# Optimization experiments

Hardware: AMD Instinct MI355X
Metric: run time of the kernel (lower is better)

## Reference

```python
import jax, jax.numpy as jnp
import numpy as np

N_LAYERS = 6
N_HEADS = 16
HIDDEN = 1024
HEAD = HIDDEN // N_HEADS  # 64
FFWD = 4096
VOCAB = 32000
WIN = 512
EMBED = 128
BATCH = 4
NEG_INF = -1.0e9


def layer_norm(x, bias, scale, eps=1e-6):
    m = jnp.mean(x, axis=-1, keepdims=True)
    v = jnp.mean(jnp.square(x - m), axis=-1, keepdims=True)
    return (x - m) * jax.lax.rsqrt(v + eps) * scale + bias


def setup_inputs() -> dict:
    key = jax.random.key(0)
    ks = jax.random.split(key, 16)

    def rn(k, shape):
        return 0.1 * jax.random.normal(k, shape, jnp.float32)

    return {
        "x_input": jax.random.randint(ks[0], (BATCH, WIN), 0, VOCAB),
        "prev_inputs": jax.random.normal(ks[1], (N_LAYERS, BATCH, WIN, HIDDEN), jnp.float32),
        "W_emb_dec": rn(ks[2], (VOCAB, EMBED)),
        "W_dec_lin": rn(ks[3], (EMBED, HIDDEN)),
        "p_decoder": rn(ks[4], (HIDDEN, VOCAB)),
        "p_d_q": rn(ks[5], (N_LAYERS, HIDDEN, HIDDEN)),
        "p_d_k": rn(ks[6], (N_LAYERS, HIDDEN, HIDDEN)),
        "p_d_v": rn(ks[7], (N_LAYERS, HIDDEN, HIDDEN)),
        "p_d_c": rn(ks[8], (N_LAYERS, HIDDEN, HIDDEN)),
        "p_d_ff1": rn(ks[9], (N_LAYERS, HIDDEN, FFWD)),
        "p_d_ff2": rn(ks[10], (N_LAYERS, FFWD, HIDDEN)),
        "b_d_ff1": jnp.zeros((N_LAYERS, FFWD), jnp.float32),
        "b_d_ff2": jnp.zeros((N_LAYERS, HIDDEN), jnp.float32),
        "b_d_bias_1": jnp.zeros((N_LAYERS, HIDDEN), jnp.float32),
        "b_d_bias_2": jnp.zeros((N_LAYERS, HIDDEN), jnp.float32),
        "b_d_scale_1": jnp.ones((N_LAYERS, HIDDEN), jnp.float32),
        "b_d_scale_2": jnp.ones((N_LAYERS, HIDDEN), jnp.float32),
        "x_emb_pos_dec": rn(ks[11], (N_LAYERS, 2 * WIN, HIDDEN)),
    }


def reference(x_input, prev_inputs, W_emb_dec, W_dec_lin, p_decoder,
              p_d_q, p_d_k, p_d_v, p_d_c, p_d_ff1, p_d_ff2,
              b_d_ff1, b_d_ff2, b_d_bias_1, b_d_bias_2,
              b_d_scale_1, b_d_scale_2, x_emb_pos_dec):
    L = x_input.shape[1]
    # token embedding (scaled by 1/sqrt(hidden)) then linear to hidden
    tok = W_emb_dec[x_input] * (HIDDEN ** -0.5)        # [B, L, E]
    h0 = jnp.einsum('ble,eh->blh', tok, W_dec_lin)     # [B, L, H]

    mask_len = L + WIN
    mask = NEG_INF * (1.0 - jnp.tril(jnp.ones((mask_len, mask_len), jnp.float32)))

    def split_heads(x):
        b, t, _ = x.shape
        return x.reshape(b, t, N_HEADS, HEAD).transpose(0, 2, 1, 3)  # [B, nH, T, d]

    def layer_fn(layer_input, p):
        Wq, Wk, Wv, Wc, Wf1, Wf2, bf1, bf2, b1, s1, b2, s2, pos, prev = p
        # concat cached window with current input, add positional embedding
        x = pos[None] + jnp.concatenate([prev, layer_input], axis=1)  # [B, 2W, H]
        q = split_heads(x @ Wq) * (HEAD ** -0.5)
        k = split_heads(x @ Wk)
        v = split_heads(x @ Wv)
        scores = jnp.einsum('bhqd,bhkd->bhqk', q, k) + mask
        alphas = jax.nn.softmax(scores, axis=-1)
        o = jnp.einsum('bhqk,bhkd->bhqd', alphas, v)
        o = o.transpose(0, 2, 1, 3).reshape(x.shape)  # combine heads
        attn = o @ Wc
        # var_type == 'norm_add': residual + LN(sublayer)
        x_self = x + layer_norm(attn, b1, s1)
        ff = jnp.maximum(x_self @ Wf1 + bf1, 0.0) @ Wf2 + bf2
        y = x_self + layer_norm(ff, b2, s2)
        new = y[:, WIN:, :]  # drop the cached-window positions
        return new, new

    params = (p_d_q, p_d_k, p_d_v, p_d_c, p_d_ff1, p_d_ff2,
              b_d_ff1, b_d_ff2, b_d_bias_1, b_d_scale_1,
              b_d_bias_2, b_d_scale_2, x_emb_pos_dec, prev_inputs)
    _, dec_outputs = jax.lax.scan(layer_fn, h0, params)  # [n_layers, B, L, H]
    dec_logits = jnp.einsum('blh,hv->blv', dec_outputs[-1], p_decoder)
    return (dec_logits, dec_outputs)
```

## Files before the change

kernel.cpp:

```cpp
#include <hip/hip_runtime.h>
#include <hip/hip_bf16.h>

#define NL   6
#define NH   16
#define HID  1024
#define HD   64
#define FFW  4096
#define VOC  32000
#define WINN 512
#define EMB  128
#define NB   4
#define TT   1024

typedef __attribute__((ext_vector_type(8))) _Float16 f16x8;
typedef __attribute__((ext_vector_type(8))) short    b16x8;
typedef __attribute__((ext_vector_type(4))) float    f32x4;

__device__ __forceinline__ ushort f2b(float f) {
    __hip_bfloat16 h = __float2bfloat16(f);
    return *reinterpret_cast<ushort*>(&h);
}
__device__ __forceinline__ void split16(float f, ushort& hb, ushort& lb) {
    _Float16 h = (_Float16)f;
    _Float16 l = (_Float16)((f - (float)h) * 2048.0f);
    hb = __builtin_bit_cast(ushort, h);
    lb = __builtin_bit_cast(ushort, l);
}
__device__ __forceinline__ void gload16(const void* g, void* l) {
    __builtin_amdgcn_global_load_lds(
        (const __attribute__((address_space(1))) unsigned int*)g,
        (__attribute__((address_space(3))) unsigned int*)l, 16, 0, 0);
}

__global__ __launch_bounds__(256) void embed_kernel(
    const int* __restrict__ xin, const float* __restrict__ Wemb,
    const float* __restrict__ Wlin, float* __restrict__ h0)
{
    int row = blockIdx.x;
    int tok = xin[row];
    __shared__ float tk[EMB];
    if (threadIdx.x < EMB) tk[threadIdx.x] = Wemb[tok * EMB + threadIdx.x] * 0.03125f;
    __syncthreads();
    for (int j = 0; j < 4; ++j) {
        int c = threadIdx.x + 256 * j;
        float acc = 0.f;
        for (int e = 0; e < EMB; ++e) acc += tk[e] * Wlin[e * HID + c];
        h0[(long)row * HID + c] = acc;
    }
}

__global__ __launch_bounds__(256) void build_x_kernel(
    const float* __restrict__ pos, const float* __restrict__ prev,
    const float* __restrict__ cur, float* __restrict__ x,
    ushort* __restrict__ xh, ushort* __restrict__ xl)
{
    int i4 = blockIdx.x * blockDim.x + threadIdx.x;
    if (i4 >= NB * TT * HID / 4) return;
    int h4 = i4 % (HID / 4);
    int bt = i4 / (HID / 4);
    int t = bt % TT, b = bt / TT;
    float4 p = ((const float4*)pos)[t * (HID / 4) + h4];
    float4 s;
    if (t < WINN) s = ((const float4*)prev)[(long)(b * WINN + t) * (HID / 4) + h4];
    else          s = ((const float4*)cur)[(long)(b * WINN + (t - WINN)) * (HID / 4) + h4];
    float4 r; r.x = p.x + s.x; r.y = p.y + s.y; r.z = p.z + s.z; r.w = p.w + s.w;
    ((float4*)x)[i4] = r;
    ushort4 uh, ul;
    split16(r.x, uh.x, ul.x); split16(r.y, uh.y, ul.y);
    split16(r.z, uh.z, ul.z); split16(r.w, uh.w, ul.w);
    ((ushort4*)xh)[i4] = uh;
    ((ushort4*)xl)[i4] = ul;
}

__global__ __launch_bounds__(256) void wsplit_kernel(
    const float* __restrict__ W, ushort* __restrict__ Wth, ushort* __restrict__ Wtl,
    int K, int N)
{
    __shared__ float ts[32][33];
    int n0 = blockIdx.x * 32, k0 = blockIdx.y * 32;
    int tr = threadIdx.x >> 5, tc = threadIdx.x & 31;
#pragma unroll
    for (int j = 0; j < 4; ++j)
        ts[tr + j * 8][tc] = W[(long)(k0 + tr + j * 8) * N + n0 + tc];
    __syncthreads();
#pragma unroll
    for (int j = 0; j < 4; ++j) {
        int n = tr + j * 8;
        ushort hb, lb;
        split16(ts[tc][n], hb, lb);
        long idx = (long)(n0 + n) * K + k0 + tc;
        Wth[idx] = hb;
        Wtl[idx] = lb;
    }
}

__global__ __launch_bounds__(256) void wsplit4_kernel(
    const float* __restrict__ pq, const float* __restrict__ pk,
    const float* __restrict__ pv, const float* __restrict__ pc,
    ushort* __restrict__ wq_h, ushort* __restrict__ wq_l,
    ushort* __restrict__ wkv_h, ushort* __restrict__ wkv_l,
    ushort* __restrict__ wc_h, ushort* __restrict__ wc_l)
{
    const float* src; ushort* dh; ushort* dl;
    switch (blockIdx.z) {
        case 0:  src = pq; dh = wq_h;            dl = wq_l;            break;
        case 1:  src = pk; dh = wkv_h;           dl = wkv_l;           break;
        case 2:  src = pv; dh = wkv_h + 1048576; dl = wkv_l + 1048576; break;
        default: src = pc; dh = wc_h;            dl = wc_l;            break;
    }
    __shared__ float ts[32][33];
    int n0 = blockIdx.x * 32, k0 = blockIdx.y * 32;
    int tr = threadIdx.x >> 5, tc = threadIdx.x & 31;
#pragma unroll
    for (int j = 0; j < 4; ++j)
        ts[tr + j * 8][tc] = src[(long)(k0 + tr + j * 8) * HID + n0 + tc];
    __syncthreads();
#pragma unroll
    for (int j = 0; j < 4; ++j) {
        int n = tr + j * 8;
        ushort hb, lb;
        split16(ts[tc][n], hb, lb);
        long idx = (long)(n0 + n) * HID + k0 + tc;
        dh[idx] = hb;
        dl[idx] = lb;
    }
}

__global__ __launch_bounds__(256) void vtrans_kernel(
    const ushort* __restrict__ vh, const ushort* __restrict__ vl,
    ushort* __restrict__ vth, ushort* __restrict__ vtl, int src_stride)
{
    __shared__ ushort th[32][33], tl[32][33];
    int n0 = blockIdx.x * 32, r0 = blockIdx.y * 32;
    int tr = threadIdx.x >> 5, tc = threadIdx.x & 31;
#pragma unroll
    for (int j = 0; j < 4; ++j) {
        long g = (long)(r0 + tr + j * 8) * src_stride + n0 + tc;
        th[tr + j * 8][tc] = vh[g];
        tl[tr + j * 8][tc] = vl[g];
    }
    __syncthreads();
#pragma unroll
    for (int j = 0; j < 4; ++j) {
        long g = (long)(n0 + tr + j * 8) * (NB * TT) + r0 + tc;
        vth[g] = th[tc][tr + j * 8];
        vtl[g] = tl[tc][tr + j * 8];
    }
}

__global__ __launch_bounds__(512) void hgemm8(
    const ushort* __restrict__ Ah, const ushort* __restrict__ Al,
    const ushort* __restrict__ Bh, const ushort* __restrict__ Bl,
    ushort* __restrict__ Chh, ushort* __restrict__ Cll,
    float* __restrict__ Cf0, float* __restrict__ Cf1,
    float* __restrict__ Cf2, float* __restrict__ Cf3,
    int M, int N, int K_stride, int Ksub,
    float scale, const float* __restrict__ bias, int relu, int amap)
{
    __shared__ __align__(16) ushort Ash[128 * 32];
    __shared__ __align__(16) ushort Asl[128 * 32];
    __shared__ __align__(16) ushort Bsh[128 * 32];
    __shared__ __align__(16) ushort Bsl[128 * 32];
    const int tid  = threadIdx.x;
    const int rb   = blockIdx.y * 128;
    const int cb   = blockIdx.x * 128;
    const int z    = blockIdx.z;
    const int k_off = z * Ksub;
    const int wave = tid >> 6, lane = tid & 63;
    const int wr   = (wave >> 2) * 64;
    const int wc   = (wave & 3) * 32;
    const int lr   = lane & 15;
    const int kh   = lane >> 4;

    const int lrow = lane >> 2;
    const int lkc  = (lane & 3) * 8;
    int gra = rb + wave * 16 + lrow;
    long marow = amap ? (long)((gra >> 9) * 1024 + 512 + (gra & 511)) : (long)gra;
    const ushort* gA_h = Ah + marow * K_stride + k_off + lkc;
    const ushort* gA_l = Al + marow * K_stride + k_off + lkc;
    const ushort* gB_h = Bh + (long)(cb + wave * 16 + lrow) * K_stride + k_off + lkc;
    const ushort* gB_l = Bl + (long)(cb + wave * 16 + lrow) * K_stride + k_off + lkc;
    ushort* lA_h = Ash + wave * 512;
    ushort* lA_l = Asl + wave * 512;
    ushort* lB_h = Bsh + wave * 512;
    ushort* lB_l = Bsl + wave * 512;

    int aoff[4], boff[2];
#pragma unroll
    for (int m = 0; m < 4; ++m) aoff[m] = (wr + m * 16 + lr) * 32 + kh * 8;
#pragma unroll
    for (int n = 0; n < 2; ++n) boff[n] = (wc + n * 16 + lr) * 32 + kh * 8;

    f32x4 accH[4][2], accL[4][2];
#pragma unroll
    for (int m = 0; m < 4; ++m)
#pragma unroll
        for (int n = 0; n < 2; ++n) {
            accH[m][n] = (f32x4){0.f, 0.f, 0.f, 0.f};
            accL[m][n] = (f32x4){0.f, 0.f, 0.f, 0.f};
        }

    for (int k0 = 0; k0 < Ksub; k0 += 32) {
        __syncthreads();
        gload16(gA_h + k0, lA_h);
        gload16(gA_l + k0, lA_l);
        gload16(gB_h + k0, lB_h);
        gload16(gB_l + k0, lB_l);
        __syncthreads();
        f16x8 afh[4], afl[4], bfh[2], bfl[2];
#pragma unroll
        for (int m = 0; m < 4; ++m) {
            afh[m] = *(const f16x8*)(Ash + aoff[m]);
            afl[m] = *(const f16x8*)(Asl + aoff[m]);
        }
#pragma unroll
        for (int n = 0; n < 2; ++n) {
            bfh[n] = *(const f16x8*)(Bsh + boff[n]);
            bfl[n] = *(const f16x8*)(Bsl + boff[n]);
        }
#pragma unroll
        for (int m = 0; m < 4; ++m)
#pragma unroll
            for (int n = 0; n < 2; ++n) {
                accH[m][n] = __builtin_amdgcn_mfma_f32_16x16x32_f16(afh[m], bfh[n], accH[m][n], 0, 0, 0);
                accL[m][n] = __builtin_amdgcn_mfma_f32_16x16x32_f16(afh[m], bfl[n], accL[m][n], 0, 0, 0);
                accL[m][n] = __builtin_amdgcn_mfma_f32_16x16x32_f16(afl[m], bfh[n], accL[m][n], 0, 0, 0);
            }
    }

    if (Cf0) {
        float* __restrict__ Cf = (z == 0) ? Cf0 : (z == 1) ? Cf1 : (z == 2) ? Cf2 : Cf3;
        const float* bias_eff = (z == 0) ? bias : nullptr;
#pragma unroll
        for (int m = 0; m < 4; ++m) {
            int row0 = rb + wr + m * 16 + kh * 4;
#pragma unroll
            for (int n = 0; n < 2; ++n) {
                int col = cb + wc + n * 16 + lr;
                float bv = bias_eff ? bias_eff[col] : 0.f;
#pragma unroll
                for (int r = 0; r < 4; ++r) {
                    float v = (accH[m][n][r] + accL[m][n][r] * (1.f / 2048.f)) * scale + bv;
                    if (relu) v = fmaxf(v, 0.f);
                    Cf[(long)(row0 + r) * N + col] = v;
                }
            }
        }
    } else {
#pragma unroll
        for (int m = 0; m < 4; ++m) {
            int row0 = rb + wr + m * 16 + kh * 4;
#pragma unroll
            for (int n = 0; n < 2; ++n) {
                int col = cb + wc + n * 16 + lr;
                float bv = bias ? bias[col] : 0.f;
#pragma unroll
                for (int r = 0; r < 4; ++r) {
                    float v = (accH[m][n][r] + accL[m][n][r] * (1.f / 2048.f)) * scale + bv;
                    if (relu) v = fmaxf(v, 0.f);
                    long idx = (long)(row0 + r) * N + col;
                    ushort hb, lb; split16(v, hb, lb);
                    Chh[idx] = hb; Cll[idx] = lb;
                }
            }
        }
    }
}

__global__ __launch_bounds__(256) void fattn_mfma(
    const float* __restrict__ qa, const float* __restrict__ qb,
    const float* __restrict__ qc, const float* __restrict__ qd,
    const ushort* __restrict__ kbh, const ushort* __restrict__ kbl, int kstr,
    const ushort* __restrict__ vth, const ushort* __restrict__ vtl,
    ushort* __restrict__ oh, ushort* __restrict__ ol)
{
    __shared__ __align__(16) ushort ksh[64 * 72];
    __shared__ __align__(16) ushort ksl[64 * 72];
    __shared__ __align__(16) ushort vsh[64 * 72];
    __shared__ __align__(16) ushort vsl[64 * 72];
    const int qt = blockIdx.x, h = blockIdx.y, b = blockIdx.z;
    const int tid = threadIdx.x;
    const int wave = tid >> 6, lane = tid & 63;
    const int lr = lane & 15, kg4 = lane >> 4;
    const int qbase = b * WINN + qt * 64;

    f16x8 qfh[2], qfl[2];
#pragma unroll
    for (int c = 0; c < 2; ++c) {
        long ga = (long)(qbase + wave * 16 + lr) * HID + h * HD + c * 32 + kg4 * 8;
        float4 a0 = *(const float4*)(qa + ga);
        float4 a1 = *(const float4*)(qa + ga + 4);
        float4 b0 = *(const float4*)(qb + ga);
        float4 b1 = *(const float4*)(qb + ga + 4);
        float4 c0 = *(const float4*)(qc + ga);
        float4 c1 = *(const float4*)(qc + ga + 4);
        float4 d0 = *(const float4*)(qd + ga);
        float4 d1 = *(const float4*)(qd + ga + 4);
        float qv[8] = {a0.x + b0.x + c0.x + d0.x, a0.y + b0.y + c0.y + d0.y,
                       a0.z + b0.z + c0.z + d0.z, a0.w + b0.w + c0.w + d0.w,
                       a1.x + b1.x + c1.x + d1.x, a1.y + b1.y + c1.y + d1.y,
                       a1.z + b1.z + c1.z + d1.z, a1.w + b1.w + c1.w + d1.w};
        ushort uh[8], ul[8];
#pragma unroll
        for (int j = 0; j < 8; ++j) split16(qv[j], uh[j], ul[j]);
        qfh[c] = *(const f16x8*)uh;
        qfl[c] = *(const f16x8*)ul;
    }

    f32x4 accOH[4], accOL[4];
#pragma unroll
    for (int d = 0; d < 4; ++d) {
        accOH[d] = (f32x4){0.f, 0.f, 0.f, 0.f};
        accOL[d] = (f32x4){0.f, 0.f, 0.f, 0.f};
    }
    float mrow[4], lrow[4];
#pragma unroll
    for (int r = 0; r < 4; ++r) { mrow[r] = -3.0e38f; lrow[r] = 0.f; }

    const int sr = tid >> 2;
    const int sd = (tid & 3) * 16;

    uint4 rk0, rk1, rk2, rk3, rv0, rv1, rv2, rv3;
    {
        long gk = (long)(b * TT + sr) * kstr + h * HD + sd;
        rk0 = *(const uint4*)(kbh + gk); rk1 = *(const uint4*)(kbh + gk + 8);
        rk2 = *(const uint4*)(kbl + gk); rk3 = *(const uint4*)(kbl + gk + 8);
        long gv = (long)(h * HD + sr) * (NB * TT) + b * TT + sd;
        rv0 = *(const uint4*)(vth + gv); rv1 = *(const uint4*)(vth + gv + 8);
        rv2 = *(const uint4*)(vtl + gv); rv3 = *(const uint4*)(vtl + gv + 8);
    }

    const int ktmax = 9 + qt;
    for (int kt = 0; kt < ktmax; ++kt) {
        __syncthreads();
        *(uint4*)(ksh + sr * 72 + sd) = rk0;
        *(uint4*)(ksh + sr * 72 + sd + 8) = rk1;
        *(uint4*)(ksl + sr * 72 + sd) = rk2;
        *(uint4*)(ksl + sr * 72 + sd + 8) = rk3;
        *(uint4*)(vsh + sr * 72 + sd) = rv0;
        *(uint4*)(vsh + sr * 72 + sd + 8) = rv1;
        *(uint4*)(vsl + sr * 72 + sd) = rv2;
        *(uint4*)(vsl + sr * 72 + sd + 8) = rv3;
        __syncthreads();

        f32x4 sH[4], sL[4];
#pragma unroll
        for (int n = 0; n < 4; ++n) {
            sH[n] = (f32x4){0.f, 0.f, 0.f, 0.f};
            sL[n] = (f32x4){0.f, 0.f, 0.f, 0.f};
        }
#pragma unroll
        for (int c = 0; c < 2; ++c) {
#pragma unroll
            for (int n = 0; n < 4; ++n) {
                int ad = (n * 16 + lr) * 72 + c * 32 + kg4 * 8;
                f16x8 bh = *(const f16x8*)(ksh + ad);
                f16x8 bl = *(const f16x8*)(ksl + ad);
                sH[n] = __builtin_amdgcn_mfma_f32_16x16x32_f16(qfh[c], bh, sH[n], 0, 0, 0);
                sL[n] = __builtin_amdgcn_mfma_f32_16x16x32_f16(qfh[c], bl, sL[n], 0, 0, 0);
                sL[n] = __builtin_amdgcn_mfma_f32_16x16x32_f16(qfl[c], bh, sL[n], 0, 0, 0);
            }
        }

        if (kt + 1 < ktmax) {
            long gk = (long)(b * TT + (kt + 1) * 64 + sr) * kstr + h * HD + sd;
            rk0 = *(const uint4*)(kbh + gk); rk1 = *(const uint4*)(kbh + gk + 8);
            rk2 = *(const uint4*)(kbl + gk); rk3 = *(const uint4*)(kbl + gk + 8);
            long gv = (long)(h * HD + sr) * (NB * TT) + b * TT + (kt + 1) * 64 + sd;
            rv0 = *(const uint4*)(vth + gv); rv1 = *(const uint4*)(vth + gv + 8);
            rv2 = *(const uint4*)(vtl + gv); rv3 = *(const uint4*)(vtl + gv + 8);
        }

        float S[4][4];
#pragma unroll
        for (int n = 0; n < 4; ++n)
#pragma unroll
            for (int r = 0; r < 4; ++r)
                S[n][r] = sH[n][r] + sL[n][r] * (1.f / 2048.f);

        if (kt == ktmax - 1) {
#pragma unroll
            for (int r = 0; r < 4; ++r) {
                int qi = WINN + qt * 64 + wave * 16 + kg4 * 4 + r;
#pragma unroll
                for (int n = 0; n < 4; ++n) {
                    int kg = kt * 64 + n * 16 + lr;
                    if (kg > qi) S[n][r] = -1e9f;
                }
            }
        }

#pragma unroll
        for (int r = 0; r < 4; ++r) {
            float mx = fmaxf(fmaxf(S[0][r], S[1][r]), fmaxf(S[2][r], S[3][r]));
            mx = fmaxf(mx, __shfl_xor(mx, 1));
            mx = fmaxf(mx, __shfl_xor(mx, 2));
            mx = fmaxf(mx, __shfl_xor(mx, 4));
            mx = fmaxf(mx, __shfl_xor(mx, 8));
            float mnew = fmaxf(mrow[r], mx);
            float alpha = __expf(mrow[r] - mnew);
            float rs = 0.f;
#pragma unroll
            for (int n = 0; n < 4; ++n) { S[n][r] = __expf(S[n][r] - mnew); rs += S[n][r]; }
            rs += __shfl_xor(rs, 1);
            rs += __shfl_xor(rs, 2);
            rs += __shfl_xor(rs, 4);
            rs += __shfl_xor(rs, 8);
            lrow[r] = lrow[r] * alpha + rs;
            mrow[r] = mnew;
#pragma unroll
            for (int d = 0; d < 4; ++d) { accOH[d][r] *= alpha; accOL[d][r] *= alpha; }
        }

        __syncthreads();
#pragma unroll
        for (int n = 0; n < 4; ++n)
#pragma unroll
            for (int r = 0; r < 4; ++r) {
                ushort hb, lb;
                split16(S[n][r], hb, lb);
                int ad = (wave * 16 + kg4 * 4 + r) * 72 + n * 16 + lr;
                ksh[ad] = hb;
                ksl[ad] = lb;
            }
        f16x8 pfh[2], pfl[2];
#pragma unroll
        for (int c = 0; c < 2; ++c) {
            int ad = (wave * 16 + lr) * 72 + c * 32 + kg4 * 8;
            pfh[c] = *(const f16x8*)(ksh + ad);
            pfl[c] = *(const f16x8*)(ksl + ad);
        }
#pragma unroll
        for (int c = 0; c < 2; ++c) {
#pragma unroll
            for (int d = 0; d < 4; ++d) {
                int ad = (d * 16 + lr) * 72 + c * 32 + kg4 * 8;
                f16x8 vh = *(const f16x8*)(vsh + ad);
                f16x8 vl = *(const f16x8*)(vsl + ad);
                accOH[d] = __builtin_amdgcn_mfma_f32_16x16x32_f16(pfh[c], vh, accOH[d], 0, 0, 0);
                accOL[d] = __builtin_amdgcn_mfma_f32_16x16x32_f16(pfh[c], vl, accOL[d], 0, 0, 0);
                accOL[d] = __builtin_amdgcn_mfma_f32_16x16x32_f16(pfl[c], vh, accOL[d], 0, 0, 0);
            }
        }
    }

#pragma unroll
    for (int r = 0; r < 4; ++r) {
        float inv = 1.f / lrow[r];
        long rowb = (long)(qbase + wave * 16 + kg4 * 4 + r) * HID + h * HD + lr;
#pragma unroll
        for (int d = 0; d < 4; ++d) {
            float v = (accOH[d][r] + accOL[d][r] * (1.f / 2048.f)) * inv;
            ushort hb, lb;
            split16(v, hb, lb);
            oh[rowb + d * 16] = hb;
            ol[rowb + d * 16] = lb;
        }
    }
}

__global__ __launch_bounds__(256) void transp_kernel(
    const float* __restrict__ W, ushort* __restrict__ Wt, int K, int N)
{
    __shared__ float ts[32][33];
    int n0 = blockIdx.x * 32, k0 = blockIdx.y * 32;
    int tr = threadIdx.x >> 5, tc = threadIdx.x & 31;
#pragma unroll
    for (int j = 0; j < 4; ++j)
        ts[tr + j * 8][tc] = W[(long)(k0 + tr + j * 8) * N + n0 + tc];
    __syncthreads();
#pragma unroll
    for (int j = 0; j < 4; ++j) {
        int n = tr + j * 8;
        Wt[(long)(n0 + n) * K + k0 + tc] = f2b(ts[tc][n]);
    }
}

__global__ __launch_bounds__(256) void mfma_gemm(
    const ushort* __restrict__ A, const ushort* __restrict__ Bt,
    float* __restrict__ Cf, int M, int N, int K)
{
    __shared__ __align__(16) ushort As[128 * 32];
    __shared__ __align__(16) ushort Bs[128 * 32];
    const int tid  = threadIdx.x;
    const int ntm  = M >> 7;
    const int nbx  = gridDim.x;
    const int nwg  = nbx * gridDim.y;
    const int bid  = blockIdx.y * nbx + blockIdx.x;
    const int cpx  = nwg >> 3;
    const int swz  = (bid & 7) * cpx + (bid >> 3);
    const int rb   = (swz % ntm) * 128;
    const int cb   = (swz / ntm) * 128;
    const int wave = tid >> 6, lane = tid & 63;
    const int wr   = (wave >> 1) * 64;
    const int wc   = (wave & 1) * 64;
    const int lr   = lane & 15;
    const int kh   = lane >> 4;

    const int lrow = lane >> 2;
    const int lkc  = (lane & 3) * 8;
    const ushort* gA0 = A + (long)(rb + wave * 32 + lrow) * K + lkc;
    const ushort* gA1 = A + (long)(rb + wave * 32 + 16 + lrow) * K + lkc;
    const ushort* gB0 = Bt + (long)(cb + wave * 32 + lrow) * K + lkc;
    const ushort* gB1 = Bt + (long)(cb + wave * 32 + 16 + lrow) * K + lkc;
    ushort* lA0 = As + wave * 1024;
    ushort* lA1 = As + wave * 1024 + 512;
    ushort* lB0 = Bs + wave * 1024;
    ushort* lB1 = Bs + wave * 1024 + 512;

    int aoff[4], boff[4];
#pragma unroll
    for (int m = 0; m < 4; ++m) aoff[m] = (wr + m * 16 + lr) * 32 + kh * 8;
#pragma unroll
    for (int n = 0; n < 4; ++n) boff[n] = (wc + n * 16 + lr) * 32 + kh * 8;

    f32x4 acc[4][4];
#pragma unroll
    for (int m = 0; m < 4; ++m)
#pragma unroll
        for (int n = 0; n < 4; ++n)
            acc[m][n] = (f32x4){0.f, 0.f, 0.f, 0.f};

    for (int k0 = 0; k0 < K; k0 += 32) {
        __syncthreads();
        gload16(gA0 + k0, lA0);
        gload16(gA1 + k0, lA1);
        gload16(gB0 + k0, lB0);
        gload16(gB1 + k0, lB1);
        __syncthreads();
        b16x8 af[4], bfr[4];
#pragma unroll
        for (int m = 0; m < 4; ++m) af[m] = *(const b16x8*)(As + aoff[m]);
#pragma unroll
        for (int n = 0; n < 4; ++n) bfr[n] = *(const b16x8*)(Bs + boff[n]);
#pragma unroll
        for (int m = 0; m < 4; ++m)
#pragma unroll
            for (int n = 0; n < 4; ++n)
                acc[m][n] = __builtin_amdgcn_mfma_f32_16x16x32_bf16(af[m], bfr[n], acc[m][n], 0, 0, 0);
    }

#pragma unroll
    for (int m = 0; m < 4; ++m) {
        int row0 = rb + wr + m * 16 + kh * 4;
#pragma unroll
        for (int n = 0; n < 4; ++n) {
            int col = cb + wc + n * 16 + lr;
#pragma unroll
            for (int r = 0; r < 4; ++r)
                Cf[(long)(row0 + r) * N + col] = acc[m][n][r];
        }
    }
}

__global__ __launch_bounds__(256) void ln_res_kernel(
    const float* __restrict__ t, const float* __restrict__ t2,
    const float* __restrict__ t3, const float* __restrict__ t4,
    const float* __restrict__ res, float* __restrict__ out,
    ushort* __restrict__ outh, ushort* __restrict__ outl, ushort* __restrict__ outb,
    const float* __restrict__ bias, const float* __restrict__ scale, int res_map)
{
    int r = blockIdx.x;
    int tid = threadIdx.x;
    long rr = res_map ? (long)((r >> 9) * 1024 + 512 + (r & 511)) : (long)r;
    float4 v = ((const float4*)(t + (long)r * HID))[tid];
    if (t2) {
        float4 w = ((const float4*)(t2 + (long)r * HID))[tid];
        v.x += w.x; v.y += w.y; v.z += w.z; v.w += w.w;
    }
    if (t3) {
        float4 w = ((const float4*)(t3 + (long)r * HID))[tid];
        v.x += w.x; v.y += w.y; v.z += w.z; v.w += w.w;
    }
    if (t4) {
        float4 w = ((const float4*)(t4 + (long)r * HID))[tid];
        v.x += w.x; v.y += w.y; v.z += w.z; v.w += w.w;
    }
    __shared__ float red[4];
    float s = v.x + v.y + v.z + v.w;
    for (int off = 32; off > 0; off >>= 1) s += __shfl_xor(s, off);
    if ((tid & 63) == 0) red[tid >> 6] = s;
    __syncthreads();
    float mean = (red[0] + red[1] + red[2] + red[3]) * (1.f / HID);
    __syncthreads();
    float dx = v.x - mean, dy = v.y - mean, dz = v.z - mean, dw = v.w - mean;
    float qs = dx * dx + dy * dy + dz * dz + dw * dw;
    for (int off = 32; off > 0; off >>= 1) qs += __shfl_xor(qs, off);
    if ((tid & 63) == 0) red[tid >> 6] = qs;
    __syncthreads();
    float var = (red[0] + red[1] + red[2] + red[3]) * (1.f / HID);
    float rs = rsqrtf(var + 1e-6f);
    float4 rv = ((const float4*)(res + rr * HID))[tid];
    float4 sc4 = ((const float4*)scale)[tid];
    float4 b4  = ((const float4*)bias)[tid];
    float4 o4;
    o4.x = rv.x + dx * rs * sc4.x + b4.x;
    o4.y = rv.y + dy * rs * sc4.y + b4.y;
    o4.z = rv.z + dz * rs * sc4.z + b4.z;
    o4.w = rv.w + dw * rs * sc4.w + b4.w;
    ((float4*)(out + (long)r * HID))[tid] = o4;
    if (outh) {
        ushort4 uh, ul;
        split16(o4.x, uh.x, ul.x); split16(o4.y, uh.y, ul.y);
        split16(o4.z, uh.z, ul.z); split16(o4.w, uh.w, ul.w);
        ((ushort4*)(outh + (long)r * HID))[tid] = uh;
        ((ushort4*)(outl + (long)r * HID))[tid] = ul;
    }
    if (outb) {
        ushort4 u; u.x = f2b(o4.x); u.y = f2b(o4.y); u.z = f2b(o4.z); u.w = f2b(o4.w);
        ((ushort4*)(outb + (long)r * HID))[tid] = u;
    }
}

extern "C" void kernel_launch(void* const* d_in, const int* in_sizes, int n_in,
                              void* d_out, int out_size, void* d_ws, size_t ws_size,
                              hipStream_t stream)
{
    const int*   x_input = (const int*)  d_in[0];
    const float* prev    = (const float*)d_in[1];
    const float* Wemb    = (const float*)d_in[2];
    const float* Wlin    = (const float*)d_in[3];
    const float* pdec    = (const float*)d_in[4];
    const float* pq      = (const float*)d_in[5];
    const float* pk      = (const float*)d_in[6];
    const float* pv      = (const float*)d_in[7];
    const float* pc      = (const float*)d_in[8];
    const float* pf1     = (const float*)d_in[9];
    const float* pf2     = (const float*)d_in[10];
    const float* bf1     = (const float*)d_in[11];
    const float* bf2     = (const float*)d_in[12];
    const float* b1      = (const float*)d_in[13];
    const float* b2      = (const float*)d_in[14];
    const float* s1      = (const float*)d_in[15];
    const float* s2      = (const float*)d_in[16];
    const float* pos     = (const float*)d_in[17];

    float* outp   = (float*)d_out;
    float* logits = outp;
    float* dec    = outp + (long)2048 * VOC;

    char* base = (char*)d_ws;
    float*  x_f   = (float*) (base + 0);
    ushort* x_hi  = (ushort*)(base + 16777216);
    ushort* x_lo  = (ushort*)(base + 25165824);
    ushort* kv_hi = (ushort*)(base + 33554432);
    ushort* kv_lo = (ushort*)(base + 50331648);
    ushort* vt_hi = (ushort*)(base + 67108864);
    ushort* vt_lo = (ushort*)(base + 75497472);
    ushort* o_hi  = (ushort*)(base + 83886080);
    ushort* o_lo  = (ushort*)(base + 88080384);
    float*  t0a   = (float*) (base + 92274688);
    float*  h0    = t0a;
    float*  qa    = t0a;
    float*  t0b   = (float*) (base + 100663296);
    float*  qb    = t0b;
    float*  xs    = (float*) (base + 109051904);
    ushort* xs_hi = (ushort*)(base + 117440512);
    ushort* xs_lo = (ushort*)(base + 121634816);
    ushort* wq_hi = (ushort*)(base + 125829120);
    ushort* wq_lo = (ushort*)(base + 127926272);
    ushort* wkv_hi= (ushort*)(base + 130023424);
    ushort* wkv_lo= (ushort*)(base + 134217728);
    ushort* wc_hi = (ushort*)(base + 138412032);
    ushort* wc_lo = (ushort*)(base + 140509184);
    ushort* wf1_hi= (ushort*)(base + 142606336);
    ushort* wf1_lo= (ushort*)(base + 150994944);
    ushort* wf2_hi= (ushort*)(base + 159383552);
    ushort* wf2_lo= (ushort*)(base + 167772160);
    float*  t0c   = (float*) (base + 67108864);
    float*  t0d   = (float*) (base + 75497472);
    float*  qc    = (float*) (base + 109051904);
    float*  qd    = (float*) (base + 117440512);
    ushort* ff1_hi= (ushort*)(base + 33554432);
    ushort* ff1_lo= (ushort*)(base + 50331648);
    ushort* decb  = (ushort*)(base + 83886080);
    ushort* wdect = (ushort*)(base + 0);

    embed_kernel<<<NB * WINN, 256, 0, stream>>>(x_input, Wemb, Wlin, h0);

    for (int l = 0; l < NL; ++l) {
        const float* cur = (l == 0) ? h0 : (dec + (long)(l - 1) * 2097152);
        build_x_kernel<<<(NB * TT * HID / 4) / 256, 256, 0, stream>>>(
            pos + (long)l * TT * HID, prev + (long)l * NB * WINN * HID, cur,
            x_f, x_hi, x_lo);

        wsplit4_kernel<<<dim3(32, 32, 4), 256, 0, stream>>>(
            pq + (long)l * HID * HID, pk + (long)l * HID * HID,
            pv + (long)l * HID * HID, pc + (long)l * HID * HID,
            wq_hi, wq_lo, wkv_hi, wkv_lo, wc_hi, wc_lo);
        wsplit_kernel<<<dim3(FFW / 32, HID / 32), 256, 0, stream>>>(
            pf1 + (long)l * HID * FFW, wf1_hi, wf1_lo, HID, FFW);
        wsplit_kernel<<<dim3(HID / 32, FFW / 32), 256, 0, stream>>>(
            pf2 + (long)l * FFW * HID, wf2_hi, wf2_lo, FFW, HID);

        hgemm8<<<dim3(2048 / 128, (NB * TT) / 128, 1), 512, 0, stream>>>(
            x_hi, x_lo, wkv_hi, wkv_lo, kv_hi, kv_lo,
            nullptr, nullptr, nullptr, nullptr,
            NB * TT, 2048, HID, HID, 1.f, nullptr, 0, 0);
        hgemm8<<<dim3(HID / 128, (NB * WINN) / 128, 4), 512, 0, stream>>>(
            x_hi, x_lo, wq_hi, wq_lo, nullptr, nullptr, qa, qb, qc, qd,
            NB * WINN, HID, HID, 256, 0.125f, nullptr, 0, 1);
        vtrans_kernel<<<dim3(HID / 32, (NB * TT) / 32), 256, 0, stream>>>(
            kv_hi + 1024, kv_lo + 1024, vt_hi, vt_lo, 2048);

        fattn_mfma<<<dim3(WINN / 64, NH, NB), 256, 0, stream>>>(
            qa, qb, qc, qd, kv_hi, kv_lo, 2048, vt_hi, vt_lo, o_hi, o_lo);

        hgemm8<<<dim3(HID / 128, (NB * WINN) / 128, 4), 512, 0, stream>>>(
            o_hi, o_lo, wc_hi, wc_lo, nullptr, nullptr, t0a, t0b, t0c, t0d,
            NB * WINN, HID, HID, 256, 1.f, nullptr, 0, 0);
        ln_res_kernel<<<NB * WINN, 256, 0, stream>>>(
            t0a, t0b, t0c, t0d, x_f, xs, xs_hi, xs_lo, nullptr,
            b1 + l * HID, s1 + l * HID, 1);

        hgemm8<<<dim3(FFW / 128, (NB * WINN) / 128, 1), 512, 0, stream>>>(
            xs_hi, xs_lo, wf1_hi, wf1_lo, ff1_hi, ff1_lo,
            nullptr, nullptr, nullptr, nullptr,
            NB * WINN, FFW, HID, HID, 1.f, bf1 + l * FFW, 1, 0);
        hgemm8<<<dim3(HID / 128, (NB * WINN) / 128, 4), 512, 0, stream>>>(
            ff1_hi, ff1_lo, wf2_hi, wf2_lo, nullptr, nullptr, t0a, t0b, t0c, t0d,
            NB * WINN, HID, FFW, 1024, 1.f, bf2 + l * HID, 0, 0);
        ln_res_kernel<<<NB * WINN, 256, 0, stream>>>(
            t0a, t0b, t0c, t0d, xs, dec + (long)l * 2097152, nullptr, nullptr,
            (l == NL - 1) ? decb : nullptr, b2 + l * HID, s2 + l * HID, 0);
    }

    transp_kernel<<<dim3(VOC / 32, HID / 32), 256, 0, stream>>>(pdec, wdect, HID, VOC);
    mfma_gemm<<<dim3(VOC / 128, (NB * WINN) / 128), 256, 0, stream>>>(
        decb, wdect, logits, NB * WINN, VOC, HID);
}
```

Baseline: 2.392 ms.

## Use exp2 softmax with lazy rescaling, MFMA priority hints, and merged FF weight splits

Folds log2(e) into the Q scaling so the attention softmax can use exp2f. It also adds lazy max rescaling: the running max and accumulators are rescaled only when a new row max exceeds the old one by a threshold. MFMA blocks are wrapped in s_setprio to favour matrix issue. The two FF weight split kernels are merged into one launch. Lazy rescaling skips per-tile alpha multiplies, at the cost of possibly larger exponent values in fp16 P.

New measurement: 2.431 ms. About the same (+1.6%).

```diff
diff --git a/kernel.cpp b/kernel.cpp
--- a/kernel.cpp
+++ b/kernel.cpp
@@ -72,28 +72,6 @@
     ((ushort4*)xl)[i4] = ul;
 }
 
-__global__ __launch_bounds__(256) void wsplit_kernel(
-    const float* __restrict__ W, ushort* __restrict__ Wth, ushort* __restrict__ Wtl,
-    int K, int N)
-{
-    __shared__ float ts[32][33];
-    int n0 = blockIdx.x * 32, k0 = blockIdx.y * 32;
-    int tr = threadIdx.x >> 5, tc = threadIdx.x & 31;
-#pragma unroll
-    for (int j = 0; j < 4; ++j)
-        ts[tr + j * 8][tc] = W[(long)(k0 + tr + j * 8) * N + n0 + tc];
-    __syncthreads();
-#pragma unroll
-    for (int j = 0; j < 4; ++j) {
-        int n = tr + j * 8;
-        ushort hb, lb;
-        split16(ts[tc][n], hb, lb);
-        long idx = (long)(n0 + n) * K + k0 + tc;
-        Wth[idx] = hb;
-        Wtl[idx] = lb;
-    }
-}
-
 __global__ __launch_bounds__(256) void wsplit4_kernel(
     const float* __restrict__ pq, const float* __restrict__ pk,
     const float* __restrict__ pv, const float* __restrict__ pc,
@@ -121,6 +99,36 @@
         ushort hb, lb;
         split16(ts[tc][n], hb, lb);
         long idx = (long)(n0 + n) * HID + k0 + tc;
+        dh[idx] = hb;
+        dl[idx] = lb;
+    }
+}
+
+__global__ __launch_bounds__(256) void wsplitff_kernel(
+    const float* __restrict__ pf1, const float* __restrict__ pf2,
+    ushort* __restrict__ f1h, ushort* __restrict__ f1l,
+    ushort* __restrict__ f2h, ushort* __restrict__ f2l)
+{
+    const float* W; ushort* dh; ushort* dl; int K, N, n0, k0;
+    if (blockIdx.z == 0) {
+        W = pf1; dh = f1h; dl = f1l; K = HID; N = FFW;
+        n0 = blockIdx.x * 32; k0 = blockIdx.y * 32;
+    } else {
+        W = pf2; dh = f2h; dl = f2l; K = FFW; N = HID;
+        n0 = blockIdx.y * 32; k0 = blockIdx.x * 32;
+    }
+    __shared__ float ts[32][33];
+    int tr = threadIdx.x >> 5, tc = threadIdx.x & 31;
+#pragma unroll
+    for (int j = 0; j < 4; ++j)
+        ts[tr + j * 8][tc] = W[(long)(k0 + tr + j * 8) * N + n0 + tc];
+    __syncthreads();
+#pragma unroll
+    for (int j = 0; j < 4; ++j) {
+        int n = tr + j * 8;
+        ushort hb, lb;
+        split16(ts[tc][n], hb, lb);
+        long idx = (long)(n0 + n) * K + k0 + tc;
         dh[idx] = hb;
         dl[idx] = lb;
     }
@@ -267,6 +275,7 @@
     }
 }
 
+#define RTHR 11.0f
 __global__ __launch_bounds__(256) void fattn_mfma(
     const float* __restrict__ qa, const float* __restrict__ qb,
     const float* __restrict__ qc, const float* __restrict__ qd,
@@ -349,6 +358,7 @@
             sH[n] = (f32x4){0.f, 0.f, 0.f, 0.f};
             sL[n] = (f32x4){0.f, 0.f, 0.f, 0.f};
         }
+        __builtin_amdgcn_s_setprio(1);
 #pragma unroll
         for (int c = 0; c < 2; ++c) {
 #pragma unroll
@@ -361,6 +371,7 @@
                 sL[n] = __builtin_amdgcn_mfma_f32_16x16x32_f16(qfl[c], bh, sL[n], 0, 0, 0);
             }
         }
+        __builtin_amdgcn_s_setprio(0);
 
         if (kt + 1 < ktmax) {
             long gk = (long)(b * TT + (kt + 1) * 64 + sr) * kstr + h * HD + sd;
@@ -390,26 +401,39 @@
             }
         }
 
+        float mx[4];
 #pragma unroll
         for (int r = 0; r < 4; ++r) {
-            float mx = fmaxf(fmaxf(S[0][r], S[1][r]), fmaxf(S[2][r], S[3][r]));
-            mx = fmaxf(mx, __shfl_xor(mx, 1));
-            mx = fmaxf(mx, __shfl_xor(mx, 2));
-            mx = fmaxf(mx, __shfl_xor(mx, 4));
-            mx = fmaxf(mx, __shfl_xor(mx, 8));
-            float mnew = fmaxf(mrow[r], mx);
-            float alpha = __expf(mrow[r] - mnew);
+            float m0 = fmaxf(fmaxf(S[0][r], S[1][r]), fmaxf(S[2][r], S[3][r]));
+            m0 = fmaxf(m0, __shfl_xor(m0, 1));
+            m0 = fmaxf(m0, __shfl_xor(m0, 2));
+            m0 = fmaxf(m0, __shfl_xor(m0, 4));
+            m0 = fmaxf(m0, __shfl_xor(m0, 8));
+            mx[r] = m0;
+        }
+        bool need = (mx[0] > mrow[0] + RTHR) || (mx[1] > mrow[1] + RTHR) ||
+                    (mx[2] > mrow[2] + RTHR) || (mx[3] > mrow[3] + RTHR);
+        if (__ballot(need)) {
+#pragma unroll
+            for (int r = 0; r < 4; ++r) {
+                float mnew = fmaxf(mrow[r], mx[r]);
+                float alpha = exp2f(mrow[r] - mnew);
+                lrow[r] *= alpha;
+                mrow[r] = mnew;
+#pragma unroll
+                for (int d = 0; d < 4; ++d) { accOH[d][r] *= alpha; accOL[d][r] *= alpha; }
+            }
+        }
+#pragma unroll
+        for (int r = 0; r < 4; ++r) {
             float rs = 0.f;
 #pragma unroll
-            for (int n = 0; n < 4; ++n) { S[n][r] = __expf(S[n][r] - mnew); rs += S[n][r]; }
+            for (int n = 0; n < 4; ++n) { S[n][r] = exp2f(S[n][r] - mrow[r]); rs += S[n][r]; }
             rs += __shfl_xor(rs, 1);
             rs += __shfl_xor(rs, 2);
             rs += __shfl_xor(rs, 4);
             rs += __shfl_xor(rs, 8);
-            lrow[r] = lrow[r] * alpha + rs;
-            mrow[r] = mnew;
-#pragma unroll
-            for (int d = 0; d < 4; ++d) { accOH[d][r] *= alpha; accOL[d][r] *= alpha; }
+            lrow[r] += rs;
         }
 
         __syncthreads();
@@ -430,6 +454,7 @@
             pfh[c] = *(const f16x8*)(ksh + ad);
             pfl[c] = *(const f16x8*)(ksl + ad);
         }
+        __builtin_amdgcn_s_setprio(1);
 #pragma unroll
         for (int c = 0; c < 2; ++c) {
 #pragma unroll
@@ -442,6 +467,7 @@
                 accOL[d] = __builtin_amdgcn_mfma_f32_16x16x32_f16(pfl[c], vh, accOL[d], 0, 0, 0);
             }
         }
+        __builtin_amdgcn_s_setprio(0);
     }
 
 #pragma unroll
@@ -688,10 +714,9 @@
             pq + (long)l * HID * HID, pk + (long)l * HID * HID,
             pv + (long)l * HID * HID, pc + (long)l * HID * HID,
             wq_hi, wq_lo, wkv_hi, wkv_lo, wc_hi, wc_lo);
-        wsplit_kernel<<<dim3(FFW / 32, HID / 32), 256, 0, stream>>>(
-            pf1 + (long)l * HID * FFW, wf1_hi, wf1_lo, HID, FFW);
-        wsplit_kernel<<<dim3(HID / 32, FFW / 32), 256, 0, stream>>>(
-            pf2 + (long)l * FFW * HID, wf2_hi, wf2_lo, FFW, HID);
+        wsplitff_kernel<<<dim3(128, 32, 2), 256, 0, stream>>>(
+            pf1 + (long)l * HID * FFW, pf2 + (long)l * FFW * HID,
+            wf1_hi, wf1_lo, wf2_hi, wf2_lo);
 
         hgemm8<<<dim3(2048 / 128, (NB * TT) / 128, 1), 512, 0, stream>>>(
             x_hi, x_lo, wkv_hi, wkv_lo, kv_hi, kv_lo,
@@ -699,7 +724,7 @@
             NB * TT, 2048, HID, HID, 1.f, nullptr, 0, 0);
         hgemm8<<<dim3(HID / 128, (NB * WINN) / 128, 4), 512, 0, stream>>>(
             x_hi, x_lo, wq_hi, wq_lo, nullptr, nullptr, qa, qb, qc, qd,
-            NB * WINN, HID, HID, 256, 0.125f, nullptr, 0, 1);
+            NB * WINN, HID, HID, 256, 0.125f * 1.44269504088896f, nullptr, 0, 1);
         vtrans_kernel<<<dim3(HID / 32, (NB * TT) / 32), 256, 0, stream>>>(
             kv_hi + 1024, kv_lo + 1024, vt_hi, vt_lo, 2048);
 
```
